# Kernel optimization log

Hardware: AMD Instinct MI355X
Metric: run time of the kernel (lower is better)

The kernel has to match this reference:

```python
import jax, jax.numpy as jnp
import numpy as np

B, S, D, H = 4, 2048, 128, 8  # batch, seq, embed_dim (= head dim), num_heads
STD = 0.01


def setup_inputs() -> dict:
    key = jax.random.key(0)
    ks = jax.random.split(key, 24)
    n = lambda k, shape, std=1.0: std * jax.random.normal(k, shape, dtype=jnp.float32)
    inp = {
        'Q': n(ks[0], (B, S, D)), 'K': n(ks[1], (B, S, D)), 'V': n(ks[2], (B, S, D)),
        'Q_position': n(ks[3], (B, S, D)), 'K_position': n(ks[4], (B, S, D)), 'V_position': n(ks[5], (B, S, D)),
        # torch Linear layout: weight [out, in], bias [out]
        'WQ_w': n(ks[6], (H * D, D), STD), 'WQ_b': n(ks[7], (H * D,), STD),
        'WK_w': n(ks[8], (H * D, D), STD), 'WK_b': n(ks[9], (H * D,), STD),
        'WV_w': n(ks[10], (H * D, D), STD), 'WV_b': n(ks[11], (H * D,), STD),
        'WQP_w': n(ks[12], (H * D, D), STD), 'WQP_b': n(ks[13], (H * D,), STD),
        'WKP_w': n(ks[14], (H * D, D), STD), 'WKP_b': n(ks[15], (H * D,), STD),
        'WVP_w': n(ks[16], (H * D, D), STD), 'WVP_b': n(ks[17], (H * D,), STD),
        'qlin_w': n(ks[18], (D, H * D), STD), 'qlin_b': n(ks[19], (D,), STD),
        'vlin_w': n(ks[20], (D, H * D), STD), 'vlin_b': n(ks[21], (D,), STD),
        'ln_g': jnp.ones((D,), jnp.float32), 'ln_b': jnp.zeros((D,), jnp.float32),
    }
    return inp


def _heads(x, w, b):
    # [B,S,D] @ [D, H*D] -> [B,H,S,D]
    bsz, slen = x.shape[0], x.shape[1]
    y = x @ w.T + b
    return y.reshape(bsz, slen, H, D).transpose(0, 2, 1, 3)


def _layer_norm(x, g, b, eps=1e-5):
    mu = jnp.mean(x, axis=-1, keepdims=True)
    var = jnp.mean(jnp.square(x - mu), axis=-1, keepdims=True)
    return (x - mu) * jax.lax.rsqrt(var + eps) * g + b


def reference(Q, K, V, Q_position, K_position, V_position,
              WQ_w, WQ_b, WK_w, WK_b, WV_w, WV_b,
              WQP_w, WQP_b, WKP_w, WKP_b, WVP_w, WVP_b,
              qlin_w, qlin_b, vlin_w, vlin_b, ln_g, ln_b):
    scale = 1.0 / float(np.sqrt(D))
    q = _heads(Q, WQ_w, WQ_b)            # [B,H,S,D]
    k = _heads(K, WK_w, WK_b)
    v = _heads(V, WV_w, WV_b)
    qp = _heads(Q_position, WQP_w, WQP_b)
    kp = _heads(K_position, WKP_w, WKP_b)
    scores = (jnp.einsum('bhqd,bhkd->bhqk', q, k)
              + jnp.einsum('bhqd,bhkd->bhqk', qp, kp)) * scale
    attn = jax.nn.softmax(scores, axis=-1)
    ctx = jnp.einsum('bhqk,bhkd->bhqd', attn, v)
    ctx = ctx.transpose(0, 2, 1, 3).reshape(Q.shape[0], -1, H * D)
    out = _layer_norm(ctx @ qlin_w.T + qlin_b + Q, ln_g, ln_b)
    v_flat = v.transpose(0, 2, 1, 3).reshape(Q.shape[0], -1, H * D)
    v_out = v_flat @ vlin_w.T + vlin_b
    return out, v_out
```

## Files before the change

kernel.cpp:

```cpp
#include <hip/hip_runtime.h>

typedef __attribute__((ext_vector_type(8))) __bf16 bf16x8;
typedef __attribute__((ext_vector_type(4))) float f32x4;
typedef __attribute__((ext_vector_type(16))) float f32x16;
typedef __attribute__((ext_vector_type(4))) unsigned int u32x4;
typedef __attribute__((ext_vector_type(8))) int i32x8;
typedef unsigned char u8;

#define DEV static __device__ __forceinline__

constexpr int B_ = 4, S_ = 2048, H_ = 8;
constexpr float C_LOG = 0.08838834764831845f * 1.4426950408889634f / 1024.0f;

constexpr size_t WS_Q2   = 0;
constexpr size_t WS_K2   = WS_Q2  + (size_t)B_*H_*S_*256;
constexpr size_t WS_VT   = WS_K2  + (size_t)B_*H_*S_*256;
constexpr size_t WS_CTX  = WS_VT  + (size_t)B_*H_*S_*128;
constexpr size_t WS_WBF  = WS_CTX + (size_t)B_*S_*1024*2;
constexpr size_t WS_QLIN = WS_WBF + (size_t)5*1024*128*2;
constexpr size_t WS_WCMB = WS_QLIN + (size_t)128*1024*2;
constexpr size_t WS_BCMB = WS_WCMB + (size_t)128*128*2;
constexpr size_t WS_XBF  = WS_BCMB + 1024;

DEV __bf16 f2b(float f) {
    unsigned u = __builtin_bit_cast(unsigned, f);
    unsigned r = u + 0x7fffu + ((u >> 16) & 1u);
    unsigned short h = (unsigned short)(r >> 16);
    return __builtin_bit_cast(__bf16, h);
}

DEV float fexp2a(float x) {
    float t = fmaf(x, 8388608.f, 1065096966.f);
    int i = (int)t;
    return __builtin_bit_cast(float, i);
}

DEV unsigned pk2(float a, float b) {
    unsigned r;
    asm("v_cvt_pk_bf16_f32 %0, %1, %2" : "=v"(r) : "v"(a), "v"(b));
    return r;
}

DEV bf16x8 cvt8(f32x4 a, f32x4 b) {
    u32x4 u{pk2(a[0], a[1]), pk2(a[2], a[3]), pk2(b[0], b[1]), pk2(b[2], b[3])};
    return __builtin_bit_cast(bf16x8, u);
}

DEV unsigned pkf8(float a, float b) {
    return (unsigned)__builtin_amdgcn_cvt_pk_fp8_f32(a, b, 0, false);
}
DEV unsigned pkf8h(unsigned old, float a, float b) {
    return (unsigned)__builtin_amdgcn_cvt_pk_fp8_f32(a, b, (int)old, true);
}
DEV u8 f2f8(float a) { return (u8)(pkf8(a, a) & 0xffu); }

DEV i32x8 ld32_8al(const u8* p) {
    long a = *(const long*)p, b = *(const long*)(p + 8);
    long c = *(const long*)(p + 16), d = *(const long*)(p + 24);
    i32x8 r;
    r[0] = (int)a; r[1] = (int)(a >> 32);
    r[2] = (int)b; r[3] = (int)(b >> 32);
    r[4] = (int)c; r[5] = (int)(c >> 32);
    r[6] = (int)d; r[7] = (int)(d >> 32);
    return r;
}

DEV f32x16 mfma64(i32x8 a, i32x8 b, f32x16 c) {
    return __builtin_amdgcn_mfma_scale_f32_32x32x64_f8f6f4(
        a, b, c, 0, 0, 0, 0x7f7f7f7f, 0, 0x7f7f7f7f);
}

__global__ __launch_bounds__(256) void k_prep(const float* wq, const float* wk,
                                              const float* wv, const float* wqp,
                                              const float* wkp, const float* qlin,
                                              const float* vlin_w, const float* wv_b,
                                              const float* vlin_b,
                                              const float* Qin, const float* Kin,
                                              const float* Vin, const float* QPin,
                                              const float* KPin, char* ws) {
    int bx = blockIdx.x, t = threadIdx.x;
    if (bx < 384) {
        __bf16* wbf = (__bf16*)(ws + WS_WBF);
        __bf16* qlb = (__bf16*)(ws + WS_QLIN);
        size_t i8 = ((size_t)bx * 256 + t) * 8;
        if (i8 < 655360) {
            int p = (int)(i8 >> 17);
            size_t e = i8 & 131071;
            int n = (int)(e >> 7), k = (int)(e & 127);
            const float* src = p == 0 ? wq : p == 1 ? wk : p == 2 ? wv : p == 3 ? wqp : wkp;
            f32x4 a = *(const f32x4*)(src + e);
            f32x4 b = *(const f32x4*)(src + e + 4);
            size_t off = (size_t)p * 131072 + ((size_t)((n >> 5) * 16 + (k >> 3))) * 256 + (n & 31) * 8;
            *(bf16x8*)(wbf + off) = cvt8(a, b);
        } else {
            size_t e = i8 - 655360;
            int n = (int)(e >> 10), k = (int)(e & 1023);
            f32x4 a = *(const f32x4*)(qlin + e);
            f32x4 b = *(const f32x4*)(qlin + e + 4);
            size_t off = ((size_t)((n >> 5) * 128 + (k >> 3))) * 256 + (n & 31) * 8;
            *(bf16x8*)(qlb + off) = cvt8(a, b);
        }
    } else if (bx < 896) {
        __bf16* wc = (__bf16*)(ws + WS_WCMB);
        int bx2 = bx - 384;
        int j = bx2 & 127, ic = bx2 >> 7;
        int il = t >> 3, part = t & 7;
        int i = ic * 32 + il;
        const float* vr = vlin_w + (size_t)i * 1024 + part * 128;
        const float* wp = wv + (size_t)part * 128 * 128 + j;
        float s = 0.f;
        #pragma unroll 4
        for (int kk = 0; kk < 32; ++kk) {
            f32x4 a = *(const f32x4*)(vr + kk * 4);
            s += a[0] * wp[(kk * 4 + 0) * 128] + a[1] * wp[(kk * 4 + 1) * 128]
               + a[2] * wp[(kk * 4 + 2) * 128] + a[3] * wp[(kk * 4 + 3) * 128];
        }
        s += __shfl_xor(s, 1);
        s += __shfl_xor(s, 2);
        s += __shfl_xor(s, 4);
        if (part == 0)
            wc[((size_t)ic * 16 + (j >> 3)) * 256 + il * 8 + (j & 7)] = f2b(s);
    } else if (bx < 900) {
        float* bc = (float*)(ws + WS_BCMB);
        int m0 = (bx - 896) * 32;
        int i = m0 + (t >> 3), part = t & 7;
        float s = 0.f;
        const float* vr = vlin_w + (size_t)i * 1024 + part * 128;
        const float* br = wv_b + part * 128;
        #pragma unroll 8
        for (int kk = 0; kk < 32; ++kk) {
            f32x4 a = *(const f32x4*)(vr + kk * 4);
            f32x4 b = *(const f32x4*)(br + kk * 4);
            s += a[0]*b[0] + a[1]*b[1] + a[2]*b[2] + a[3]*b[3];
        }
        s += __shfl_xor(s, 1);
        s += __shfl_xor(s, 2);
        s += __shfl_xor(s, 4);
        if (part == 0) bc[i] = s + vlin_b[i];
    } else {
        __bf16* xbf = (__bf16*)(ws + WS_XBF);
        size_t c = (size_t)(bx - 900) * 256 + t;
        int p = (int)(c >> 17);
        size_t e = (c & 131071) * 8;
        const float* src = p == 0 ? Qin : p == 1 ? Kin : p == 2 ? Vin : p == 3 ? QPin : KPin;
        f32x4 a = *(const f32x4*)(src + e);
        f32x4 b = *(const f32x4*)(src + e + 4);
        *(bf16x8*)(xbf + (size_t)p * 1048576 + e) = cvt8(a, b);
    }
}

__global__ __launch_bounds__(256) void k_proj(const float* bq, const float* bk,
                                              const float* bv, const float* bqp,
                                              const float* bkp, char* ws, float* out) {
    int bx = blockIdx.x, t = threadIdx.x;
    int lane = t & 63, w = t >> 6, lo = lane & 31, hi = lane >> 5;
    int xcd = bx & 7, seq = bx >> 3;
    u8* q2  = (u8*)(ws + WS_Q2);
    u8* k2  = (u8*)(ws + WS_K2);
    u8* vbT = (u8*)(ws + WS_VT);
    const __bf16* xbf = (const __bf16*)(ws + WS_XBF);
    if (seq < 320) {
        int T = (seq & ~7) + xcd;
        int nq = seq & 7;
        int p = T >> 6, mt = T & 63;
        int m0 = mt * 128 + w * 32, n0 = nq * 128;
        const float* bias = p == 0 ? bq  : p == 1 ? bk  : p == 2 ? bv  : p == 3 ? bqp  : bkp;
        const __bf16* wb = (const __bf16*)(ws + WS_WBF) + (size_t)p * 131072;
        f32x16 acc[4];
        #pragma unroll
        for (int g = 0; g < 4; ++g)
            #pragma unroll
            for (int i = 0; i < 16; ++i) acc[g][i] = 0.f;
        const __bf16* arow = xbf + (size_t)p * 1048576 + (size_t)(m0 + lo) * 128;
        #pragma unroll
        for (int ks = 0; ks < 8; ++ks) {
            bf16x8 af = *(const bf16x8*)(arow + ks * 16 + hi * 8);
            #pragma unroll
            for (int g = 0; g < 4; ++g) {
                bf16x8 bf = *(const bf16x8*)&wb[((size_t)(nq * 4 + g) * 16 + ks * 2 + hi) * 256 + lo * 8];
                acc[g] = __builtin_amdgcn_mfma_f32_32x32x16_bf16(af, bf, acc[g], 0, 0, 0);
            }
        }
        int b = m0 >> 11, s0w = m0 & 2047;
        if (p == 2) {
            #pragma unroll
            for (int g = 0; g < 4; ++g) {
                int n = n0 + g * 32 + lo, h = n >> 7, d = n & 127;
                float bn = bias[n];
                u8* dp = vbT + (((size_t)(b * H_ + h)) * 128 + d) * (size_t)S_ + s0w + 4 * hi;
                #pragma unroll
                for (int rq = 0; rq < 4; ++rq) {
                    unsigned wd = pkf8((acc[g][rq*4+0] + bn) * 16.f,
                                       (acc[g][rq*4+1] + bn) * 16.f);
                    wd = pkf8h(wd, (acc[g][rq*4+2] + bn) * 16.f,
                                   (acc[g][rq*4+3] + bn) * 16.f);
                    *(unsigned*)&dp[rq * 8] = wd;
                }
            }
        } else {
            int off = (p == 0 || p == 1) ? 0 : 128;
            u8* dstbuf = (p == 0 || p == 3) ? q2 : k2;
            #pragma unroll
            for (int g = 0; g < 4; ++g) {
                int n = n0 + g * 32 + lo, h = n >> 7, d = n & 127;
                float bn = bias[n];
                u8* dp = dstbuf + (((size_t)(b * H_ + h)) * S_ + s0w + 4 * hi) * 256 + off + d;
                #pragma unroll
                for (int r = 0; r < 16; ++r)
                    dp[((r & 3) + 8 * (r >> 2)) * 256] = f2f8((acc[g][r] + bn) * 32.f);
            }
        }
    } else {
        int T2 = (seq - 320) * 8 + xcd;
        int m0 = T2 * 128 + w * 32;
        const __bf16* wc = (const __bf16*)(ws + WS_WCMB);
        const float*  bc = (const float*)(ws + WS_BCMB);
        f32x16 acc[4];
        #pragma unroll
        for (int g = 0; g < 4; ++g)
            #pragma unroll
            for (int i = 0; i < 16; ++i) acc[g][i] = 0.f;
        const __bf16* arow = xbf + (size_t)2 * 1048576 + (size_t)(m0 + lo) * 128;
        #pragma unroll
        for (int ks = 0; ks < 8; ++ks) {
            bf16x8 af = *(const bf16x8*)(arow + ks * 16 + hi * 8);
            #pragma unroll
            for (int g = 0; g < 4; ++g) {
                bf16x8 bf = *(const bf16x8*)&wc[((size_t)g * 16 + ks * 2 + hi) * 256 + lo * 8];
                acc[g] = __builtin_amdgcn_mfma_f32_32x32x16_bf16(af, bf, acc[g], 0, 0, 0);
            }
        }
        #pragma unroll
        for (int g = 0; g < 4; ++g) {
            int n = g * 32 + lo;
            float bn = bc[n];
            float* op = out + 1048576 + (size_t)(m0 + 4 * hi) * 128 + n;
            #pragma unroll
            for (int r = 0; r < 16; ++r)
                op[((r & 3) + 8 * (r >> 2)) * 128] = acc[g][r] + bn;
        }
    }
}

__global__ __launch_bounds__(256, 2) void k_attn(char* ws) {
    __shared__ __align__(16) u8 Kb[2][16896];
    __shared__ __align__(16) u8 Vt[2][9216];
    const u8* q2 = (const u8*)(ws + WS_Q2);
    const u8* k2 = (const u8*)(ws + WS_K2);
    const u8* vT = (const u8*)(ws + WS_VT);
    __bf16* ctxg = (__bf16*)(ws + WS_CTX);

    int bx = blockIdx.x;
    int xcd = bx & 7;
    int idx = bx >> 3;
    int bh = xcd * 4 + (idx >> 4);
    int qt = idx & 15;
    int t = threadIdx.x, lane = t & 63, w = t >> 6;
    int lo = lane & 31, hi = lane >> 5;

    const u8* k2b = k2 + (size_t)bh * S_ * 256;
    const u8* vTb = vT + (size_t)bh * 128 * S_;
    int q0 = qt * 128;
    int qrow = q0 + w * 32 + lo;

    i32x8 qf[4];
    {
        const u8* qp = q2 + ((size_t)bh * S_ + qrow) * 256 + hi * 32;
        #pragma unroll
        for (int kb = 0; kb < 4; ++kb) qf[kb] = ld32_8al(qp + kb * 64);
    }

    f32x16 ctx[4], lacc;
    #pragma unroll
    for (int i = 0; i < 4; ++i)
        #pragma unroll
        for (int j = 0; j < 16; ++j) ctx[i][j] = 0.f;
    #pragma unroll
    for (int j = 0; j < 16; ++j) lacc[j] = 0.f;

    i32x8 ones;
    #pragma unroll
    for (int j = 0; j < 8; ++j) ones[j] = 0x38383838;

    u32x4 kA[4], kB[4];
    long vA[4], vB[4];

    auto load_k = [&](u32x4* kr, int kt) __attribute__((always_inline)) {
        const u8* src = k2b + (size_t)kt * 16384 + t * 16;
        #pragma unroll
        for (int i = 0; i < 4; ++i) kr[i] = *(const u32x4*)(src + i * 4096);
    };
    auto write_k = [&](int buf, const u32x4* kr) __attribute__((always_inline)) {
        u8* dst = &Kb[buf][(t >> 4) * 264 + (t & 15) * 16];
        #pragma unroll
        for (int i = 0; i < 4; ++i) {
            u32x4 v = kr[i];
            long lo8 = (long)(((unsigned long)v[1] << 32) | v[0]);
            long hi8 = (long)(((unsigned long)v[3] << 32) | v[2]);
            *(long*)(dst + (size_t)i * 4224) = lo8;
            *(long*)(dst + (size_t)i * 4224 + 8) = hi8;
        }
    };
    auto load_v = [&](long* vr, int kt) __attribute__((always_inline)) {
        #pragma unroll
        for (int i = 0; i < 4; ++i) {
            int d = i * 32 + (t >> 3), kb = t & 7;
            vr[i] = *(const long*)(vTb + (size_t)d * S_ + kt * 64 + kb * 8);
        }
    };
    auto write_vt = [&](int buf, const long* vr) __attribute__((always_inline)) {
        #pragma unroll
        for (int i = 0; i < 4; ++i) {
            int d = i * 32 + (t >> 3), kb = t & 7;
            *(long*)&Vt[buf][d * 72 + kb * 8] = vr[i];
        }
    };
    auto body = [&](int it, const u8* kbp, const u8* vtp,
                    u32x4* kld, long* vld, const u32x4* kwr, const long* vwr,
                    int wbuf) __attribute__((always_inline)) {
        f32x16 s0, s1;
        #pragma unroll
        for (int j = 0; j < 16; ++j) { s0[j] = 0.f; s1[j] = 0.f; }
        __builtin_amdgcn_s_setprio(1);
        #pragma unroll
        for (int kb = 0; kb < 4; ++kb) {
            i32x8 a0 = ld32_8al(&kbp[lo * 264 + kb * 64 + hi * 32]);
            i32x8 a1 = ld32_8al(&kbp[(32 + lo) * 264 + kb * 64 + hi * 32]);
            s0 = mfma64(a0, qf[kb], s0);
            s1 = mfma64(a1, qf[kb], s1);
        }
        __builtin_amdgcn_s_setprio(0);

        int kt2 = it + 2 < 32 ? it + 2 : 31;
        load_k(kld, kt2);
        load_v(vld, kt2);

        #pragma unroll
        for (int j = 0; j < 16; ++j) {
            s0[j] = fexp2a(fmaf(s0[j], C_LOG, 4.0f));
            s1[j] = fexp2a(fmaf(s1[j], C_LOG, 4.0f));
        }

        unsigned d[4], e[4];
        #pragma unroll
        for (int a = 0; a < 4; ++a) {
            d[a] = pkf8h(pkf8(s0[4*a], s0[4*a+1]), s0[4*a+2], s0[4*a+3]);
            e[a] = pkf8h(pkf8(s1[4*a], s1[4*a+1]), s1[4*a+2], s1[4*a+3]);
        }
        #pragma unroll
        for (int a = 0; a < 4; ++a)
            asm("v_permlane32_swap_b32 %0, %1" : "+v"(e[a]), "+v"(d[a]));
        i32x8 pfr;
        pfr[0] = (int)d[0]; pfr[1] = (int)e[0];
        pfr[2] = (int)d[1]; pfr[3] = (int)e[1];
        pfr[4] = (int)d[2]; pfr[5] = (int)e[2];
        pfr[6] = (int)d[3]; pfr[7] = (int)e[3];

        __builtin_amdgcn_s_setprio(1);
        #pragma unroll
        for (int ds = 0; ds < 4; ++ds) {
            i32x8 va = ld32_8al(&vtp[(ds * 32 + lo) * 72 + hi * 32]);
            ctx[ds] = mfma64(va, pfr, ctx[ds]);
        }
        lacc = mfma64(ones, pfr, lacc);
        __builtin_amdgcn_s_setprio(0);

        asm volatile("s_waitcnt vmcnt(8)" ::: "memory");
        __builtin_amdgcn_sched_barrier(0);
        write_k(wbuf, kwr);
        write_vt(wbuf, vwr);
        asm volatile("s_waitcnt lgkmcnt(0)" ::: "memory");
        __builtin_amdgcn_s_barrier();
        __builtin_amdgcn_sched_barrier(0);
    };

    load_k(kA, 0);
    load_v(vA, 0);
    load_k(kB, 1);
    load_v(vB, 1);
    asm volatile("s_waitcnt vmcnt(8)" ::: "memory");
    __builtin_amdgcn_sched_barrier(0);
    write_k(0, kA);
    write_vt(0, vA);
    asm volatile("s_waitcnt lgkmcnt(0)" ::: "memory");
    __builtin_amdgcn_s_barrier();
    __builtin_amdgcn_sched_barrier(0);

    for (int it2 = 0; it2 < 16; ++it2) {
        body(it2 * 2,     &Kb[0][0], &Vt[0][0], kA, vA, kB, vB, 1);
        body(it2 * 2 + 1, &Kb[1][0], &Vt[1][0], kB, vB, kA, vA, 0);
    }

    __bf16* sc = (__bf16*)&Kb[0][0] + w * 4096;
    float inv = 1.f / (16.f * lacc[0]);
    #pragma unroll
    for (int ds = 0; ds < 4; ++ds) {
        #pragma unroll
        for (int g = 0; g < 4; ++g) {
            #pragma unroll
            for (int h2 = 0; h2 < 2; ++h2) {
                int r = g * 4 + h2 * 2;
                unsigned pv = pk2(ctx[ds][r] * inv, ctx[ds][r + 1] * inv);
                int d = ds * 32 + (r & 3) + 8 * (r >> 2) + 4 * hi;
                *(unsigned*)&sc[lo * 128 + (((d >> 3) ^ (lo & 7)) << 3) + (d & 7)] = pv;
            }
        }
    }
    {
        int b = bh >> 3, h = bh & 7;
        int qq = lane >> 1, halfd = lane & 1;
        int srow = q0 + w * 32 + qq;
        #pragma unroll
        for (int j = 0; j < 8; ++j) {
            int d8 = halfd * 8 + j;
            bf16x8 vv = *(const bf16x8*)&sc[qq * 128 + ((d8 ^ (qq & 7)) << 3)];
            *(bf16x8*)&ctxg[((size_t)(b * S_ + srow)) * 1024 + h * 128 + d8 * 8] = vv;
        }
    }
}

__global__ __launch_bounds__(256) void k_out(const float* Qin, const float* qlin_b,
                                             const float* ln_g, const float* ln_b,
                                             char* ws, float* out) {
    __shared__ f32x16 red[3][4][64];
    int t = threadIdx.x, w = t >> 6, l64 = t & 63;
    int lo = l64 & 31, hi = l64 >> 5;
    int m0 = blockIdx.x * 32;
    const __bf16* ctx = (const __bf16*)(ws + WS_CTX);
    const __bf16* qlb = (const __bf16*)(ws + WS_QLIN);
    f32x16 acc[4];
    #pragma unroll
    for (int g = 0; g < 4; ++g)
        #pragma unroll
        for (int i = 0; i < 16; ++i) acc[g][i] = 0.f;
    const __bf16* arow = ctx + (size_t)(m0 + lo) * 1024 + w * 256;
    #pragma unroll
    for (int ks = 0; ks < 16; ++ks) {
        int kb = ks * 16 + hi * 8;
        bf16x8 af = *(const bf16x8*)(arow + kb);
        int ksg = w * 16 + ks;
        #pragma unroll
        for (int g = 0; g < 4; ++g) {
            bf16x8 bf = *(const bf16x8*)&qlb[((size_t)g * 128 + ksg * 2 + hi) * 256 + lo * 8];
            acc[g] = __builtin_amdgcn_mfma_f32_32x32x16_bf16(af, bf, acc[g], 0, 0, 0);
        }
    }
    if (w > 0) {
        #pragma unroll
        for (int g = 0; g < 4; ++g) red[w - 1][g][l64] = acc[g];
    }
    __syncthreads();
    if (w > 0) return;
    #pragma unroll
    for (int v = 0; v < 3; ++v)
        #pragma unroll
        for (int g = 0; g < 4; ++g) {
            f32x16 o = red[v][g][l64];
            #pragma unroll
            for (int i = 0; i < 16; ++i) acc[g][i] += o[i];
        }
    float gb[4], bb[4], qb[4];
    #pragma unroll
    for (int g = 0; g < 4; ++g) {
        int n = g * 32 + lo;
        gb[g] = ln_g[n]; bb[g] = ln_b[n]; qb[g] = qlin_b[n];
    }
    const float* qp = Qin + (size_t)(m0 + 4 * hi) * 128;
    float* op = out + (size_t)(m0 + 4 * hi) * 128;
    #pragma unroll
    for (int r = 0; r < 16; ++r) {
        int ro = ((r & 3) + 8 * (r >> 2)) * 128;
        float x[4];
        float sum = 0.f;
        #pragma unroll
        for (int g = 0; g < 4; ++g) {
            x[g] = acc[g][r] + qb[g] + qp[ro + g * 32 + lo];
            sum += x[g];
        }
        sum += __shfl_xor(sum, 1);
        sum += __shfl_xor(sum, 2);
        sum += __shfl_xor(sum, 4);
        sum += __shfl_xor(sum, 8);
        sum += __shfl_xor(sum, 16);
        float mean = sum * (1.f / 128.f);
        float sq = 0.f;
        #pragma unroll
        for (int g = 0; g < 4; ++g) {
            float d = x[g] - mean;
            sq += d * d;
        }
        sq += __shfl_xor(sq, 1);
        sq += __shfl_xor(sq, 2);
        sq += __shfl_xor(sq, 4);
        sq += __shfl_xor(sq, 8);
        sq += __shfl_xor(sq, 16);
        float rstd = rsqrtf(sq * (1.f / 128.f) + 1e-5f);
        #pragma unroll
        for (int g = 0; g < 4; ++g)
            op[ro + g * 32 + lo] = (x[g] - mean) * rstd * gb[g] + bb[g];
    }
}

extern "C" void kernel_launch(void* const* d_in, const int* in_sizes, int n_in,
                              void* d_out, int out_size, void* d_ws, size_t ws_size,
                              hipStream_t stream) {
    (void)in_sizes; (void)n_in; (void)out_size; (void)ws_size;
    const float* Q    = (const float*)d_in[0];
    const float* K    = (const float*)d_in[1];
    const float* V    = (const float*)d_in[2];
    const float* QP   = (const float*)d_in[3];
    const float* KP   = (const float*)d_in[4];
    const float* WQw  = (const float*)d_in[6];
    const float* WQb  = (const float*)d_in[7];
    const float* WKw  = (const float*)d_in[8];
    const float* WKb  = (const float*)d_in[9];
    const float* WVw  = (const float*)d_in[10];
    const float* WVb  = (const float*)d_in[11];
    const float* WQPw = (const float*)d_in[12];
    const float* WQPb = (const float*)d_in[13];
    const float* WKPw = (const float*)d_in[14];
    const float* WKPb = (const float*)d_in[15];
    const float* qlw  = (const float*)d_in[18];
    const float* qlb  = (const float*)d_in[19];
    const float* vlw  = (const float*)d_in[20];
    const float* vlb  = (const float*)d_in[21];
    const float* lng  = (const float*)d_in[22];
    const float* lnb  = (const float*)d_in[23];
    char* ws = (char*)d_ws;
    float* out = (float*)d_out;

    k_prep<<<3460, 256, 0, stream>>>(WQw, WKw, WVw, WQPw, WKPw, qlw, vlw, WVb, vlb,
                                     Q, K, V, QP, KP, ws);
    k_proj<<<2624, 256, 0, stream>>>(WQb, WKb, WVb, WQPb, WKPb, ws, out);
    k_attn<<<512, 256, 0, stream>>>(ws);
    k_out<<<256, 256, 0, stream>>>(Q, qlb, lng, lnb, ws, out);
}
```

Before: 154.7 us.

## Split attention over key halves and merge partial sums in output kernel

Each attention block now processes half of the key sequence, doubling the grid so more blocks run concurrently across CUs. Unnormalized partial context and row sums are written to separate buffers, and the output projection kernel adds the two halves and applies normalization before its MFMA. This trades extra global traffic for the second context buffer and a shorter per-block pipeline against better occupancy.

```diff
diff --git a/kernel.cpp b/kernel.cpp
--- a/kernel.cpp
+++ b/kernel.cpp
@@ -16,11 +16,13 @@
 constexpr size_t WS_K2   = WS_Q2  + (size_t)B_*H_*S_*256;
 constexpr size_t WS_VT   = WS_K2  + (size_t)B_*H_*S_*256;
 constexpr size_t WS_CTX  = WS_VT  + (size_t)B_*H_*S_*128;
-constexpr size_t WS_WBF  = WS_CTX + (size_t)B_*S_*1024*2;
+constexpr size_t WS_CTXB = WS_CTX + (size_t)B_*S_*1024*2;
+constexpr size_t WS_WBF  = WS_CTXB+ (size_t)B_*S_*1024*2;
 constexpr size_t WS_QLIN = WS_WBF + (size_t)5*1024*128*2;
 constexpr size_t WS_WCMB = WS_QLIN + (size_t)128*1024*2;
 constexpr size_t WS_BCMB = WS_WCMB + (size_t)128*128*2;
 constexpr size_t WS_XBF  = WS_BCMB + 1024;
+constexpr size_t WS_ML   = WS_XBF  + (size_t)5*8192*128*2;
 
 DEV __bf16 f2b(float f) {
     unsigned u = __builtin_bit_cast(unsigned, f);
@@ -248,13 +250,14 @@
     const u8* q2 = (const u8*)(ws + WS_Q2);
     const u8* k2 = (const u8*)(ws + WS_K2);
     const u8* vT = (const u8*)(ws + WS_VT);
-    __bf16* ctxg = (__bf16*)(ws + WS_CTX);
 
     int bx = blockIdx.x;
     int xcd = bx & 7;
     int idx = bx >> 3;
-    int bh = xcd * 4 + (idx >> 4);
-    int qt = idx & 15;
+    int bh = xcd * 4 + (idx >> 5);
+    int rem = idx & 31;
+    int qt = rem >> 1, half = rem & 1;
+    int ktbase = half * 16;
     int t = threadIdx.x, lane = t & 63, w = t >> 6;
     int lo = lane & 31, hi = lane >> 5;
 
@@ -331,9 +334,9 @@
         }
         __builtin_amdgcn_s_setprio(0);
 
-        int kt2 = it + 2 < 32 ? it + 2 : 31;
-        load_k(kld, kt2);
-        load_v(vld, kt2);
+        int it2n = it + 2 < 16 ? it + 2 : 15;
+        load_k(kld, ktbase + it2n);
+        load_v(vld, ktbase + it2n);
 
         #pragma unroll
         for (int j = 0; j < 16; ++j) {
@@ -374,10 +377,10 @@
         __builtin_amdgcn_sched_barrier(0);
     };
 
-    load_k(kA, 0);
-    load_v(vA, 0);
-    load_k(kB, 1);
-    load_v(vB, 1);
+    load_k(kA, ktbase + 0);
+    load_v(vA, ktbase + 0);
+    load_k(kB, ktbase + 1);
+    load_v(vB, ktbase + 1);
     asm volatile("s_waitcnt vmcnt(8)" ::: "memory");
     __builtin_amdgcn_sched_barrier(0);
     write_k(0, kA);
@@ -386,13 +389,18 @@
     __builtin_amdgcn_s_barrier();
     __builtin_amdgcn_sched_barrier(0);
 
-    for (int it2 = 0; it2 < 16; ++it2) {
+    for (int it2 = 0; it2 < 8; ++it2) {
         body(it2 * 2,     &Kb[0][0], &Vt[0][0], kA, vA, kB, vB, 1);
         body(it2 * 2 + 1, &Kb[1][0], &Vt[1][0], kB, vB, kA, vA, 0);
     }
 
+    {
+        float* ml = (float*)(ws + WS_ML);
+        if (hi == 0) ml[((size_t)(half * 32 + bh)) * S_ + qrow] = lacc[0];
+    }
+
+    __bf16* ctxg = (__bf16*)(ws + (half ? WS_CTXB : WS_CTX));
     __bf16* sc = (__bf16*)&Kb[0][0] + w * 4096;
-    float inv = 1.f / (16.f * lacc[0]);
     #pragma unroll
     for (int ds = 0; ds < 4; ++ds) {
         #pragma unroll
@@ -400,7 +408,7 @@
             #pragma unroll
             for (int h2 = 0; h2 < 2; ++h2) {
                 int r = g * 4 + h2 * 2;
-                unsigned pv = pk2(ctx[ds][r] * inv, ctx[ds][r + 1] * inv);
+                unsigned pv = pk2(ctx[ds][r], ctx[ds][r + 1]);
                 int d = ds * 32 + (r & 3) + 8 * (r >> 2) + 4 * hi;
                 *(unsigned*)&sc[lo * 128 + (((d >> 3) ^ (lo & 7)) << 3) + (d & 7)] = pv;
             }
@@ -426,18 +434,43 @@
     int t = threadIdx.x, w = t >> 6, l64 = t & 63;
     int lo = l64 & 31, hi = l64 >> 5;
     int m0 = blockIdx.x * 32;
-    const __bf16* ctx = (const __bf16*)(ws + WS_CTX);
+    const __bf16* ctxA = (const __bf16*)(ws + WS_CTX);
+    const __bf16* ctxB = (const __bf16*)(ws + WS_CTXB);
     const __bf16* qlb = (const __bf16*)(ws + WS_QLIN);
+    const float* ml = (const float*)(ws + WS_ML);
+
+    int arow_i = m0 + lo;
+    int b = arow_i >> 11, s = arow_i & 2047;
+    float inv0, inv1;
+    {
+        int bh0 = b * H_ + 2 * w, bh1 = bh0 + 1;
+        float lA0 = ml[(size_t)bh0 * S_ + s], lB0 = ml[((size_t)(32 + bh0)) * S_ + s];
+        float lA1 = ml[(size_t)bh1 * S_ + s], lB1 = ml[((size_t)(32 + bh1)) * S_ + s];
+        inv0 = 1.f / (16.f * (lA0 + lB0));
+        inv1 = 1.f / (16.f * (lA1 + lB1));
+    }
+
     f32x16 acc[4];
     #pragma unroll
     for (int g = 0; g < 4; ++g)
         #pragma unroll
         for (int i = 0; i < 16; ++i) acc[g][i] = 0.f;
-    const __bf16* arow = ctx + (size_t)(m0 + lo) * 1024 + w * 256;
+    const __bf16* arowA = ctxA + (size_t)arow_i * 1024 + w * 256;
+    const __bf16* arowB = ctxB + (size_t)arow_i * 1024 + w * 256;
     #pragma unroll
     for (int ks = 0; ks < 16; ++ks) {
         int kb = ks * 16 + hi * 8;
-        bf16x8 af = *(const bf16x8*)(arow + kb);
+        float invs = (ks < 8) ? inv0 : inv1;
+        bf16x8 a8 = *(const bf16x8*)(arowA + kb);
+        bf16x8 b8 = *(const bf16x8*)(arowB + kb);
+        u32x4 u;
+        #pragma unroll
+        for (int q = 0; q < 4; ++q) {
+            float x0 = ((float)a8[2*q]   + (float)b8[2*q])   * invs;
+            float x1 = ((float)a8[2*q+1] + (float)b8[2*q+1]) * invs;
+            u[q] = pk2(x0, x1);
+        }
+        bf16x8 af = __builtin_bit_cast(bf16x8, u);
         int ksg = w * 16 + ks;
         #pragma unroll
         for (int g = 0; g < 4; ++g) {
@@ -532,6 +565,6 @@
     k_prep<<<3460, 256, 0, stream>>>(WQw, WKw, WVw, WQPw, WKPw, qlw, vlw, WVb, vlb,
                                      Q, K, V, QP, KP, ws);
     k_proj<<<2624, 256, 0, stream>>>(WQb, WKb, WVb, WQPb, WKPb, ws, out);
-    k_attn<<<512, 256, 0, stream>>>(ws);
+    k_attn<<<1024, 256, 0, stream>>>(ws);
     k_out<<<256, 256, 0, stream>>>(Q, qlb, lng, lnb, ws, out);
 }
```

After: 171.2 us. 1.11x slower.
